# Optimization experiments

Measured on AMD Instinct MI355X. Metric: run time of the kernel, lower is better.

## Reference

```python
import jax, jax.numpy as jnp
import numpy as np

T, B, E, H = 4096, 2, 1024, 16          # seq, batch, embed, heads
W = 256                                  # one-sided attention window (attention_window=512 // 2)
G = 64                                   # number of global tokens (first G positions)
D = E // H
NEG = -1e9


def _band_mask():
    # valid key position for band slot j at query t is t - W + j in [0, T)
    pos = jnp.arange(T)[:, None] - W + jnp.arange(2 * W + 1)[None, :]
    return (pos >= 0) & (pos < T)  # [T, 2W+1]


def _chunk_blocks(x):
    # x: [b, t, h, d] -> key/value blocks [b, nc, 3w, h, d]; block c covers positions [c*w - w, c*w + 2w)
    b, t, h, d = x.shape
    nc = t // W
    xp = jnp.pad(x, ((0, 0), (W, 2 * W), (0, 0), (0, 0)))
    idx = jnp.arange(nc)[:, None] * W + jnp.arange(3 * W)[None, :]
    return xp[:, idx]


def _band_qk(q, k):
    # q,k: [b,t,h,d] -> banded scores [b,t,h,2w+1] (Longformer sliding_chunks_matmul_qk)
    b, t, h, d = q.shape
    nc = t // W
    qc = q.reshape(b, nc, W, h, d)
    kb = _chunk_blocks(k)
    scores = jnp.einsum('bcxhd,bcyhd->bhcxy', qc, kb)          # y in [0, 3w)
    y_idx = jnp.arange(W)[:, None] + jnp.arange(2 * W + 1)[None, :]  # [w, 2w+1]
    band = jnp.take_along_axis(scores, y_idx[None, None, None], axis=-1)
    band = band.reshape(b, h, t, 2 * W + 1).transpose(0, 2, 1, 3)
    return jnp.where(_band_mask()[None, :, None, :], band, NEG)


def _band_pv(p, v):
    # p: [b,t,h,2w+1], v: [b,t,h,d] -> [b,t,h,d] (sliding_chunks_matmul_pv)
    b, t, h, _ = p.shape
    nc = t // W
    pb = p.transpose(0, 2, 1, 3).reshape(b, h, nc, W, 2 * W + 1)
    x = jnp.arange(W)
    y_idx = x[:, None] + jnp.arange(2 * W + 1)[None, :]
    p3 = jnp.zeros((b, h, nc, W, 3 * W), p.dtype).at[:, :, :, x[:, None], y_idx].set(pb)
    vb = _chunk_blocks(v)
    out = jnp.einsum('bhcxy,bcyhd->bcxhd', p3, vb)
    return out.reshape(b, t, h, -1)


def setup_inputs() -> dict:
    key = jax.random.key(0)
    ks = jax.random.split(key, 16)
    s = 0.02
    inp = {
        'query': jax.random.normal(ks[0], (T, B, E), jnp.float32),
        'attn_mask': jnp.concatenate([jnp.ones((B, G), jnp.int64), jnp.zeros((B, T - G), jnp.int64)], axis=1),
        'Wq': jax.random.normal(ks[1], (E, E), jnp.float32) * s, 'bq': jnp.zeros((E,), jnp.float32),
        'Wk': jax.random.normal(ks[2], (E, E), jnp.float32) * s, 'bk': jnp.zeros((E,), jnp.float32),
        'Wv': jax.random.normal(ks[3], (E, E), jnp.float32) * s, 'bv': jnp.zeros((E,), jnp.float32),
        'Wqg': jax.random.normal(ks[4], (E, E), jnp.float32) * s, 'bqg': jnp.zeros((E,), jnp.float32),
        'Wkg': jax.random.normal(ks[5], (E, E), jnp.float32) * s, 'bkg': jnp.zeros((E,), jnp.float32),
        'Wvg': jax.random.normal(ks[6], (E, E), jnp.float32) * s, 'bvg': jnp.zeros((E,), jnp.float32),
        'Wo': jax.random.normal(ks[7], (E, E), jnp.float32) * s, 'bo': jnp.zeros((E,), jnp.float32),
    }
    return inp


def reference(query, attn_mask, Wq, bq, Wk, bk, Wv, bv, Wqg, bqg, Wkg, bkg, Wvg, bvg, Wo, bo):
    del attn_mask  # structure fixed: first G tokens are global, no padding
    scaling = D ** -0.5
    x = query.transpose(1, 0, 2)                      # [b, t, e]
    q = ((x @ Wq.T + bq) * scaling).reshape(B, T, H, D)
    k = (x @ Wk.T + bk).reshape(B, T, H, D)
    v = (x @ Wv.T + bv).reshape(B, T, H, D)

    band = _band_qk(q, k)                             # [b,t,h,2w+1]
    sel_w = jnp.einsum('blhd,bshd->blhs', q, k[:, :G])  # every token attends global keys
    aw = jnp.concatenate([sel_w, band], axis=-1)
    probs = jax.nn.softmax(aw.astype(jnp.float32), axis=-1).astype(aw.dtype)

    attn = jnp.einsum('blhs,bshd->blhd', probs[..., :G], v[:, :G])
    attn = attn + _band_pv(probs[..., G:], v)         # [b,t,h,d]

    # global tokens attend everything with the *_global projections
    qg = ((x[:, :G] @ Wqg.T + bqg) * scaling).reshape(B, G, H, D)
    kg = (x @ Wkg.T + bkg).reshape(B, T, H, D)
    vg = (x @ Wvg.T + bvg).reshape(B, T, H, D)
    gs = jnp.einsum('bghd,bthd->bhgt', qg, kg)
    gp = jax.nn.softmax(gs.astype(jnp.float32), axis=-1).astype(gs.dtype)
    gout = jnp.einsum('bhgt,bthd->bghd', gp, vg)
    attn = attn.at[:, :G].set(gout)

    out = attn.reshape(B, T, E).transpose(1, 0, 2) @ Wo.T + bo  # [t, b, e]
    return out
```

## Files before the change

### kernel.cpp

```cpp
#include <hip/hip_runtime.h>
#include <hip/hip_bf16.h>

typedef unsigned short u16;
typedef __bf16 bf16x8 __attribute__((ext_vector_type(8)));
typedef float  f32x4  __attribute__((ext_vector_type(4)));

constexpr int TT = 4096;
constexpr int BBATCH = 2;
constexpr int EE = 1024;
constexpr int HH = 16;
constexpr int DD = 64;
constexpr int WQ = 256;
constexpr int GG = 64;
constexpr int NSPLIT = 8;

__device__ __forceinline__ u16 f2bf(float f) {
    union { float f; unsigned int i; } c; c.f = f;
    unsigned int x = c.i;
    return (u16)((x + 0x7fffu + ((x >> 16) & 1u)) >> 16);
}
__device__ __forceinline__ uint4 pack8(float4 a, float4 b) {
    uint4 r;
    r.x = (unsigned)f2bf(a.x) | ((unsigned)f2bf(a.y) << 16);
    r.y = (unsigned)f2bf(a.z) | ((unsigned)f2bf(a.w) << 16);
    r.z = (unsigned)f2bf(b.x) | ((unsigned)f2bf(b.y) << 16);
    r.w = (unsigned)f2bf(b.z) | ((unsigned)f2bf(b.w) << 16);
    return r;
}

__device__ __forceinline__ void g2l16(const u16* g, u16* l) {
    __builtin_amdgcn_global_load_lds(
        (const __attribute__((address_space(1))) void*)g,
        (__attribute__((address_space(3))) void*)l, 16, 0, 0);
}

__device__ __forceinline__ void xcd_swizzle(int& bx, int& by) {
    bx = blockIdx.x; by = blockIdx.y;
    if ((gridDim.y & 7) == 0) {
        const int g   = blockIdx.x + blockIdx.y * gridDim.x;
        const int idx = g >> 3;
        bx = idx % gridDim.x;
        by = (g & 7) + ((idx / gridDim.x) << 3);
    }
}

struct WPtrs { const float* p[7]; };
__global__ __launch_bounds__(256) void conv_kernel(
    WPtrs wp, const float* __restrict__ query, u16* __restrict__ wb, u16* __restrict__ xb)
{
    const size_t i8 = ((size_t)blockIdx.x * 256 + threadIdx.x) << 3;
    const size_t WTOT = (size_t)7 << 20;
    const float* src;
    u16* dst;
    if (i8 < WTOT) {
        const int which = (int)(i8 >> 20);
        src = wp.p[which] + (i8 & (((size_t)1 << 20) - 1));
        dst = wb + i8;
    } else {
        const size_t j = i8 - WTOT;
        const size_t e = j & (EE - 1);
        const size_t t = (j >> 10) & (TT - 1);
        const size_t b = j >> 22;
        src = query + (t * BBATCH + b) * EE + e;
        dst = xb + j;
    }
    const float4 f0 = *(const float4*)src;
    const float4 f1 = *(const float4*)(src + 4);
    *(uint4*)dst = pack8(f0, f1);
}

template<int C_F32, int PERMA_QG, int PERMC_TB>
__global__ __launch_bounds__(256) void gemm_kernel(
    const u16* __restrict__ A, const u16* __restrict__ W, const float* __restrict__ bias,
    void* __restrict__ Cv, float scale)
{
    const int tid = threadIdx.x, lane = tid & 63, w = tid >> 6;
    const int wm = w >> 1, wn = w & 1;
    int bx, by;
    xcd_swizzle(bx, by);
    const int m0 = by << 7, n0 = bx << 7;

    __shared__ __align__(16) u16 As[2 * 128 * 32];
    __shared__ __align__(16) u16 Bs[2 * 128 * 32];

    const int lrow = lane >> 2;
    const int lcol = (lane & 3) << 3;
    auto arow = [](int m) -> size_t {
        return PERMA_QG ? (size_t)(((m >> 6) << 12) | (m & 63)) : (size_t)m;
    };
    const u16* gA0 = A + arow(m0 + (w << 4) + lrow) * EE + lcol;
    const u16* gA1 = A + arow(m0 + 64 + (w << 4) + lrow) * EE + lcol;
    const u16* gB0 = W + (size_t)(n0 + (w << 4) + lrow) * EE + lcol;
    const u16* gB1 = gB0 + (size_t)64 * EE;
    u16* lA0 = As + (w << 9);
    u16* lA1 = As + 2048 + (w << 9);
    u16* lB0 = Bs + (w << 9);
    u16* lB1 = Bs + 2048 + (w << 9);

    f32x4 acc[4][4];
#pragma unroll
    for (int i = 0; i < 4; i++)
#pragma unroll
        for (int j = 0; j < 4; j++)
            acc[i][j] = (f32x4){0.f, 0.f, 0.f, 0.f};

    const int fr = lane & 15;
    const int fq = (lane >> 4) << 3;

    for (int k0 = 0; k0 < EE; k0 += 64) {
        g2l16(gA0 + k0, lA0);  g2l16(gA0 + k0 + 32, lA0 + 4096);
        g2l16(gA1 + k0, lA1);  g2l16(gA1 + k0 + 32, lA1 + 4096);
        g2l16(gB0 + k0, lB0);  g2l16(gB0 + k0 + 32, lB0 + 4096);
        g2l16(gB1 + k0, lB1);  g2l16(gB1 + k0 + 32, lB1 + 4096);
        __syncthreads();
#pragma unroll
        for (int p = 0; p < 2; p++) {
            bf16x8 af[4], bfv[4];
#pragma unroll
            for (int i = 0; i < 4; i++)
                af[i] = *(const bf16x8*)&As[p * 4096 + ((wm << 6) + (i << 4) + fr) * 32 + fq];
#pragma unroll
            for (int j = 0; j < 4; j++)
                bfv[j] = *(const bf16x8*)&Bs[p * 4096 + ((wn << 6) + (j << 4) + fr) * 32 + fq];
#pragma unroll
            for (int i = 0; i < 4; i++)
#pragma unroll
                for (int j = 0; j < 4; j++)
                    acc[i][j] = __builtin_amdgcn_mfma_f32_16x16x32_bf16(af[i], bfv[j], acc[i][j], 0, 0, 0);
        }
        __syncthreads();
    }

    const int colbase = n0 + (wn << 6);
    const int rowbase = m0 + (wm << 6) + ((lane >> 4) << 2);
#pragma unroll
    for (int j = 0; j < 4; j++) {
        const int col = colbase + (j << 4) + fr;
        const float bv = bias[col];
#pragma unroll
        for (int i = 0; i < 4; i++) {
#pragma unroll
            for (int r = 0; r < 4; r++) {
                const int row = rowbase + (i << 4) + r;
                const float val = (acc[i][j][r] + bv) * scale;
                const size_t dst = (size_t)(PERMC_TB ? (((row & (TT - 1)) << 1) | (row >> 12)) : row) * EE + col;
                if (C_F32) ((float*)Cv)[dst] = val;
                else       ((u16*)Cv)[dst]   = f2bf(val);
            }
        }
    }
}

struct FusedArgs { u16* out[3]; const float* bias[3]; float scale[3]; int vseg; };
template<int NSEG>
__global__ __launch_bounds__(256) void gemm_fused_kernel(
    const u16* __restrict__ A, const u16* __restrict__ W, FusedArgs fa)
{
    const int tid = threadIdx.x, lane = tid & 63, w = tid >> 6;
    const int wm = w >> 1, wn = w & 1;
    int bx, by;
    xcd_swizzle(bx, by);
    const int m0 = by << 7, n0 = bx << 7;

    __shared__ __align__(16) u16 As[2 * 128 * 32];
    __shared__ __align__(16) u16 Bs[2 * 128 * 32];

    const int lrow = lane >> 2;
    const int lcol = (lane & 3) << 3;
    const u16* gA0 = A + (size_t)(m0 + (w << 4) + lrow) * EE + lcol;
    const u16* gA1 = gA0 + (size_t)64 * EE;
    const u16* gB0 = W + (size_t)(n0 + (w << 4) + lrow) * EE + lcol;
    const u16* gB1 = gB0 + (size_t)64 * EE;
    u16* lA0 = As + (w << 9);
    u16* lA1 = As + 2048 + (w << 9);
    u16* lB0 = Bs + (w << 9);
    u16* lB1 = Bs + 2048 + (w << 9);

    f32x4 acc[4][4];
#pragma unroll
    for (int i = 0; i < 4; i++)
#pragma unroll
        for (int j = 0; j < 4; j++)
            acc[i][j] = (f32x4){0.f, 0.f, 0.f, 0.f};

    const int fr = lane & 15;
    const int fq = (lane >> 4) << 3;

    for (int k0 = 0; k0 < EE; k0 += 64) {
        g2l16(gA0 + k0, lA0);  g2l16(gA0 + k0 + 32, lA0 + 4096);
        g2l16(gA1 + k0, lA1);  g2l16(gA1 + k0 + 32, lA1 + 4096);
        g2l16(gB0 + k0, lB0);  g2l16(gB0 + k0 + 32, lB0 + 4096);
        g2l16(gB1 + k0, lB1);  g2l16(gB1 + k0 + 32, lB1 + 4096);
        __syncthreads();
#pragma unroll
        for (int p = 0; p < 2; p++) {
            bf16x8 af[4], bfv[4];
#pragma unroll
            for (int i = 0; i < 4; i++)
                af[i] = *(const bf16x8*)&As[p * 4096 + ((wm << 6) + (i << 4) + fr) * 32 + fq];
#pragma unroll
            for (int j = 0; j < 4; j++)
                bfv[j] = *(const bf16x8*)&Bs[p * 4096 + ((wn << 6) + (j << 4) + fr) * 32 + fq];
#pragma unroll
            for (int i = 0; i < 4; i++)
#pragma unroll
                for (int j = 0; j < 4; j++)
                    acc[i][j] = __builtin_amdgcn_mfma_f32_16x16x32_bf16(af[i], bfv[j], acc[i][j], 0, 0, 0);
        }
        __syncthreads();
    }

    const int seg = n0 >> 10;
    u16* outp = fa.out[seg];
    const float* bp = fa.bias[seg];
    const float scl = fa.scale[seg];
    const bool vtr = (seg == fa.vseg);

    const int colbase = n0 + (wn << 6);
    const int rowbase = m0 + (wm << 6) + ((lane >> 4) << 2);
#pragma unroll
    for (int j = 0; j < 4; j++) {
        const int col = colbase + (j << 4) + fr;
        const int cl  = col & (EE - 1);
        const float bv = bp[cl];
#pragma unroll
        for (int i = 0; i < 4; i++) {
            if (vtr) {
                const int row0 = rowbase + (i << 4);
                const int bb = row0 >> 12, t = row0 & (TT - 1);
                const int hh = cl >> 6, d = cl & 63;
                ushort4 pk;
                pk.x = f2bf((acc[i][j][0] + bv) * scl);
                pk.y = f2bf((acc[i][j][1] + bv) * scl);
                pk.z = f2bf((acc[i][j][2] + bv) * scl);
                pk.w = f2bf((acc[i][j][3] + bv) * scl);
                *(ushort4*)(outp + (((size_t)(bb * HH + hh) * DD + d) * TT + t)) = pk;
            } else {
#pragma unroll
                for (int r = 0; r < 4; r++) {
                    const int row = rowbase + (i << 4) + r;
                    outp[(size_t)row * EE + cl] = f2bf((acc[i][j][r] + bv) * scl);
                }
            }
        }
    }
}

__global__ __launch_bounds__(256) void band_attn_kernel(
    const u16* __restrict__ q, const u16* __restrict__ k, const u16* __restrict__ vt,
    u16* __restrict__ attnb)
{
    const int tid  = threadIdx.x;
    const int lane = tid & 63;
    const int w    = tid >> 6;
    const int col  = lane & 15;
    const int quad = lane >> 4;

    const int qt = blockIdx.x >> 5;
    const int bh = blockIdx.x & 31;
    const int h  = bh & (HH - 1);
    const int b  = bh >> 4;
    const int t0 = qt << 6;

    __shared__ __align__(16) u16 Ks[64][72];
    __shared__ __align__(16) u16 Vs[64][72];
    __shared__ __align__(16) u16 Ps[4][16][72];

    const size_t base   = (size_t)b * TT * EE + (size_t)h * DD;
    const size_t vtbase = (size_t)bh * DD * TT;

    const u16* qp = q + base + (size_t)(t0 + (w << 4) + col) * EE + (quad << 3);
    const bf16x8 qf0 = *(const bf16x8*)qp;
    const bf16x8 qf1 = *(const bf16x8*)(qp + 32);

    float m_i[4], l_i[4];
    f32x4 acc_o[4];
#pragma unroll
    for (int r = 0; r < 4; r++) { m_i[r] = -1e30f; l_i[r] = 0.f; }
#pragma unroll
    for (int nt = 0; nt < 4; nt++) acc_o[nt] = (f32x4){0.f, 0.f, 0.f, 0.f};

    const int c_lo = 1 + ((t0 < WQ) ? ((WQ - t0) >> 6) : 0);
    const int c_hi = min(9, 1 + ((TT + WQ - 64 - t0) >> 6));

    const int srow  = tid >> 2;
    const int spart = (tid & 3) << 4;

    auto process = [&](int kpos0, int jbase) {
        {
            const u16* ks = k + base + (size_t)(kpos0 + srow) * EE + spart;
            const u16* vs = vt + vtbase + (size_t)srow * TT + kpos0 + spart;
            const uint4 k0v = *(const uint4*)ks;
            const uint4 k1v = *(const uint4*)(ks + 8);
            const uint4 v0v = *(const uint4*)vs;
            const uint4 v1v = *(const uint4*)(vs + 8);
            *(uint4*)&Ks[srow][spart]     = k0v;
            *(uint4*)&Ks[srow][spart + 8] = k1v;
            *(uint4*)&Vs[srow][spart]     = v0v;
            *(uint4*)&Vs[srow][spart + 8] = v1v;
        }
        __syncthreads();

        f32x4 acc_s[4];
#pragma unroll
        for (int nt = 0; nt < 4; nt++) {
            const bf16x8 kf0 = *(const bf16x8*)&Ks[(nt << 4) + col][quad << 3];
            const bf16x8 kf1 = *(const bf16x8*)&Ks[(nt << 4) + col][32 + (quad << 3)];
            f32x4 s = (f32x4){0.f, 0.f, 0.f, 0.f};
            s = __builtin_amdgcn_mfma_f32_16x16x32_bf16(qf0, kf0, s, 0, 0, 0);
            s = __builtin_amdgcn_mfma_f32_16x16x32_bf16(qf1, kf1, s, 0, 0, 0);
            acc_s[nt] = s;
        }

        if (jbase >= 0) {
#pragma unroll
            for (int nt = 0; nt < 4; nt++) {
#pragma unroll
                for (int r = 0; r < 4; r++) {
                    const int jp   = jbase + (nt << 4) + col;
                    const int qrow = (w << 4) + (quad << 2) + r;
                    const bool ok  = (jp >= qrow) && (jp <= qrow + 2 * WQ);
                    if (!ok) acc_s[nt][r] = -1e30f;
                }
            }
        }

        float p_sum[4];
#pragma unroll
        for (int r = 0; r < 4; r++) {
            float mx = fmaxf(fmaxf(acc_s[0][r], acc_s[1][r]), fmaxf(acc_s[2][r], acc_s[3][r]));
#pragma unroll
            for (int off = 1; off < 16; off <<= 1) mx = fmaxf(mx, __shfl_xor(mx, off));
            const float m_new = fmaxf(m_i[r], mx);
            const float alpha = __expf(m_i[r] - m_new);
            m_i[r] = m_new;
            l_i[r] *= alpha;
#pragma unroll
            for (int nt = 0; nt < 4; nt++) acc_o[nt][r] *= alpha;
            float ps = 0.f;
#pragma unroll
            for (int nt = 0; nt < 4; nt++) {
                const float e = __expf(acc_s[nt][r] - m_new);
                acc_s[nt][r] = e;
                ps += e;
            }
            p_sum[r] = ps;
        }
#pragma unroll
        for (int r = 0; r < 4; r++) {
            float ps = p_sum[r];
#pragma unroll
            for (int off = 1; off < 16; off <<= 1) ps += __shfl_xor(ps, off);
            l_i[r] += ps;
        }

#pragma unroll
        for (int nt = 0; nt < 4; nt++)
#pragma unroll
            for (int r = 0; r < 4; r++)
                Ps[w][(quad << 2) + r][(nt << 4) + col] = f2bf(acc_s[nt][r]);

        const bf16x8 pf0 = *(const bf16x8*)&Ps[w][col][quad << 3];
        const bf16x8 pf1 = *(const bf16x8*)&Ps[w][col][32 + (quad << 3)];

#pragma unroll
        for (int nt = 0; nt < 4; nt++) {
            const bf16x8 vf0 = *(const bf16x8*)&Vs[(nt << 4) + col][quad << 3];
            const bf16x8 vf1 = *(const bf16x8*)&Vs[(nt << 4) + col][32 + (quad << 3)];
            acc_o[nt] = __builtin_amdgcn_mfma_f32_16x16x32_bf16(pf0, vf0, acc_o[nt], 0, 0, 0);
            acc_o[nt] = __builtin_amdgcn_mfma_f32_16x16x32_bf16(pf1, vf1, acc_o[nt], 0, 0, 0);
        }
        __syncthreads();
    };

    process(0, -1);
#pragma unroll 1
    for (int c = c_lo; c <= c_hi; c++) {
        const int kpos0 = t0 - WQ + ((c - 1) << 6);
        const bool edge = (c == 1) || (c == 9);
        process(kpos0, edge ? ((c - 1) << 6) : -1);
    }

    float inv[4];
#pragma unroll
    for (int r = 0; r < 4; r++) inv[r] = 1.f / l_i[r];
#pragma unroll
    for (int nt = 0; nt < 4; nt++) {
#pragma unroll
        for (int r = 0; r < 4; r++) {
            const int t = t0 + (w << 4) + (quad << 2) + r;
            attnb[base + (size_t)t * EE + (nt << 4) + col] = f2bf(acc_o[nt][r] * inv[r]);
        }
    }
}

__global__ __launch_bounds__(256) void global_attn_flash_kernel(
    const u16* __restrict__ qg, const u16* __restrict__ kg, const u16* __restrict__ vg,
    float* __restrict__ Op, float* __restrict__ Ml, float* __restrict__ Ll)
{
    const int tid  = threadIdx.x;
    const int lane = tid & 63;
    const int w    = tid >> 6;
    const int col  = lane & 15;
    const int quad = lane >> 4;

    const int s  = blockIdx.x & (NSPLIT - 1);
    const int h  = (blockIdx.x >> 3) & (HH - 1);
    const int b  = blockIdx.x >> 7;
    const int k0pos = s * (TT / NSPLIT);

    __shared__ __align__(16) u16 Qs[64][72];
    __shared__ __align__(16) u16 Ks[64][72];
    __shared__ __align__(16) u16 Vs[64][70];
    __shared__ __align__(16) u16 Ps[4][16][72];

    const size_t base = (size_t)b * TT * EE + (size_t)h * DD;

    {
        const int qr   = tid >> 2;
        const int part = (tid & 3) << 4;
        const uint4* src = (const uint4*)(qg + (size_t)(b * GG + qr) * EE + (size_t)h * DD + part);
        *(uint4*)&Qs[qr][part]     = src[0];
        *(uint4*)&Qs[qr][part + 8] = src[1];
    }

    float m_i[4], l_i[4];
    f32x4 acc_o[4];
#pragma unroll
    for (int r = 0; r < 4; r++) { m_i[r] = -1e30f; l_i[r] = 0.f; }
#pragma unroll
    for (int nt = 0; nt < 4; nt++) acc_o[nt] = (f32x4){0.f, 0.f, 0.f, 0.f};

#pragma unroll 1
    for (int cc = 0; cc < TT / NSPLIT / 64; cc++) {
        {
            const int kk   = tid >> 2;
            const int part = (tid & 3) << 4;
            const int pos  = k0pos + (cc << 6) + kk;
            const uint4* ks = (const uint4*)(kg + base + (size_t)pos * EE + part);
            const uint4* vs = (const uint4*)(vg + base + (size_t)pos * EE + part);
            const uint4 k0v = ks[0], k1v = ks[1];
            const uint4 v0v = vs[0], v1v = vs[1];
            *(uint4*)&Ks[kk][part]     = k0v;
            *(uint4*)&Ks[kk][part + 8] = k1v;
            unsigned int* vd = (unsigned int*)&Vs[kk][part];
            vd[0] = v0v.x; vd[1] = v0v.y; vd[2] = v0v.z; vd[3] = v0v.w;
            vd[4] = v1v.x; vd[5] = v1v.y; vd[6] = v1v.z; vd[7] = v1v.w;
        }
        __syncthreads();

        bf16x8 qf0 = *(const bf16x8*)&Qs[(w << 4) + col][quad << 3];
        bf16x8 qf1 = *(const bf16x8*)&Qs[(w << 4) + col][32 + (quad << 3)];
        f32x4 acc_s[4];
#pragma unroll
        for (int nt = 0; nt < 4; nt++) {
            bf16x8 kf0 = *(const bf16x8*)&Ks[(nt << 4) + col][quad << 3];
            bf16x8 kf1 = *(const bf16x8*)&Ks[(nt << 4) + col][32 + (quad << 3)];
            f32x4 sv = (f32x4){0.f, 0.f, 0.f, 0.f};
            sv = __builtin_amdgcn_mfma_f32_16x16x32_bf16(qf0, kf0, sv, 0, 0, 0);
            sv = __builtin_amdgcn_mfma_f32_16x16x32_bf16(qf1, kf1, sv, 0, 0, 0);
            acc_s[nt] = sv;
        }

        float m_c[4], p_sum[4];
#pragma unroll
        for (int r = 0; r < 4; r++) {
            float mx = fmaxf(fmaxf(acc_s[0][r], acc_s[1][r]), fmaxf(acc_s[2][r], acc_s[3][r]));
#pragma unroll
            for (int off = 1; off < 16; off <<= 1) mx = fmaxf(mx, __shfl_xor(mx, off));
            m_c[r] = mx;
        }
#pragma unroll
        for (int r = 0; r < 4; r++) {
            const float m_new = fmaxf(m_i[r], m_c[r]);
            const float alpha = __expf(m_i[r] - m_new);
            m_i[r] = m_new;
            l_i[r] *= alpha;
#pragma unroll
            for (int nt = 0; nt < 4; nt++) acc_o[nt][r] *= alpha;
            float ps = 0.f;
#pragma unroll
            for (int nt = 0; nt < 4; nt++) {
                const float e = __expf(acc_s[nt][r] - m_new);
                acc_s[nt][r] = e;
                ps += e;
            }
            p_sum[r] = ps;
        }
#pragma unroll
        for (int r = 0; r < 4; r++) {
            float ps = p_sum[r];
#pragma unroll
            for (int off = 1; off < 16; off <<= 1) ps += __shfl_xor(ps, off);
            l_i[r] += ps;
        }

#pragma unroll
        for (int nt = 0; nt < 4; nt++)
#pragma unroll
            for (int r = 0; r < 4; r++)
                Ps[w][(quad << 2) + r][(nt << 4) + col] = f2bf(acc_s[nt][r]);

        bf16x8 pf0 = *(const bf16x8*)&Ps[w][col][quad << 3];
        bf16x8 pf1 = *(const bf16x8*)&Ps[w][col][32 + (quad << 3)];
#pragma unroll
        for (int nt = 0; nt < 4; nt++) {
            union { bf16x8 v; u16 e[8]; } vf0, vf1;
#pragma unroll
            for (int j = 0; j < 8; j++) {
                vf0.e[j] = Vs[(quad << 3) + j][(nt << 4) + col];
                vf1.e[j] = Vs[32 + (quad << 3) + j][(nt << 4) + col];
            }
            acc_o[nt] = __builtin_amdgcn_mfma_f32_16x16x32_bf16(pf0, vf0.v, acc_o[nt], 0, 0, 0);
            acc_o[nt] = __builtin_amdgcn_mfma_f32_16x16x32_bf16(pf1, vf1.v, acc_o[nt], 0, 0, 0);
        }
        __syncthreads();
    }

    const size_t obase = (size_t)blockIdx.x * GG * DD;
#pragma unroll
    for (int nt = 0; nt < 4; nt++) {
#pragma unroll
        for (int r = 0; r < 4; r++) {
            const int row = (w << 4) + (quad << 2) + r;
            Op[obase + (size_t)row * DD + (nt << 4) + col] = acc_o[nt][r];
        }
    }
    if (col == 0) {
#pragma unroll
        for (int r = 0; r < 4; r++) {
            const int row = (w << 4) + (quad << 2) + r;
            Ml[blockIdx.x * GG + row] = m_i[r];
            Ll[blockIdx.x * GG + row] = l_i[r];
        }
    }
}

__global__ __launch_bounds__(256) void global_combine_kernel(
    const float* __restrict__ Op, const float* __restrict__ Ml, const float* __restrict__ Ll,
    u16* __restrict__ attnb)
{
    const int bh  = blockIdx.x;
    const int b   = bh >> 4;
    const int h   = bh & (HH - 1);
    const int row = threadIdx.x >> 2;
    const int d0  = (threadIdx.x & 3) << 4;

    float mv[NSPLIT];
    float m = -1e30f;
#pragma unroll
    for (int s = 0; s < NSPLIT; s++) {
        mv[s] = Ml[(bh * NSPLIT + s) * GG + row];
        m = fmaxf(m, mv[s]);
    }
    float l = 0.f;
    float sc[NSPLIT];
#pragma unroll
    for (int s = 0; s < NSPLIT; s++) {
        sc[s] = __expf(mv[s] - m);
        l += Ll[(bh * NSPLIT + s) * GG + row] * sc[s];
    }
    float o[16];
#pragma unroll
    for (int j = 0; j < 16; j++) o[j] = 0.f;
#pragma unroll
    for (int s = 0; s < NSPLIT; s++) {
        const float* src = Op + ((size_t)(bh * NSPLIT + s) * GG + row) * DD + d0;
        const float f = sc[s];
#pragma unroll
        for (int j = 0; j < 16; j += 4) {
            const float4 v4 = *(const float4*)(src + j);
            o[j + 0] = fmaf(v4.x, f, o[j + 0]);
            o[j + 1] = fmaf(v4.y, f, o[j + 1]);
            o[j + 2] = fmaf(v4.z, f, o[j + 2]);
            o[j + 3] = fmaf(v4.w, f, o[j + 3]);
        }
    }
    const float inv = 1.f / l;
    u16* dst = attnb + ((size_t)b * TT + row) * EE + (size_t)h * DD + d0;
#pragma unroll
    for (int j = 0; j < 16; j++) dst[j] = f2bf(o[j] * inv);
}

extern "C" void kernel_launch(void* const* d_in, const int* in_sizes, int n_in,
                              void* d_out, int out_size, void* d_ws, size_t ws_size,
                              hipStream_t stream)
{
    (void)in_sizes; (void)n_in; (void)out_size; (void)ws_size;
    const float* query = (const float*)d_in[0];
    const float* Wq  = (const float*)d_in[2];  const float* bq  = (const float*)d_in[3];
    const float* Wk  = (const float*)d_in[4];  const float* bk  = (const float*)d_in[5];
    const float* Wv  = (const float*)d_in[6];  const float* bv  = (const float*)d_in[7];
    const float* Wqg = (const float*)d_in[8];  const float* bqg = (const float*)d_in[9];
    const float* Wkg = (const float*)d_in[10]; const float* bkg = (const float*)d_in[11];
    const float* Wvg = (const float*)d_in[12]; const float* bvg = (const float*)d_in[13];
    const float* Wo  = (const float*)d_in[14]; const float* bo  = (const float*)d_in[15];

    const size_t nfull = (size_t)BBATCH * TT * EE;
    const size_t wsz   = (size_t)1 << 20;
    u16* xb    = (u16*)d_ws;
    u16* wb    = xb + nfull;
    u16* slotA = wb + 7 * wsz;
    u16* slotB = slotA + nfull;
    u16* slotC = slotB + nfull;
    u16* qg    = slotC + nfull;
    float* Op  = (float*)(qg + (size_t)BBATCH * GG * EE);
    float* Ml  = Op + (size_t)BBATCH * HH * NSPLIT * GG * DD;
    float* Ll  = Ml + (size_t)BBATCH * HH * NSPLIT * GG;
    u16* attnb = xb;

    WPtrs wp;
    wp.p[0] = Wq; wp.p[1] = Wk; wp.p[2] = Wv;
    wp.p[3] = Wkg; wp.p[4] = Wvg; wp.p[5] = Wqg; wp.p[6] = Wo;

    const dim3 blk(256);
    const dim3 gF2(16, 64);
    const dim3 gF3(24, 64);
    const dim3 gFull(8, 64);
    const dim3 gQg(8, 1);
    const float sc = 0.125f;

    conv_kernel<<<7680, blk, 0, stream>>>(wp, query, wb, xb);

    gemm_kernel<0, 1, 0><<<gQg, blk, 0, stream>>>(xb, wb + 5 * wsz, bqg, qg, sc);

    FusedArgs fa2;
    fa2.out[0] = slotA; fa2.out[1] = slotB; fa2.out[2] = nullptr;
    fa2.bias[0] = bkg;  fa2.bias[1] = bvg;  fa2.bias[2] = nullptr;
    fa2.scale[0] = 1.f; fa2.scale[1] = 1.f; fa2.scale[2] = 1.f;
    fa2.vseg = -1;
    gemm_fused_kernel<2><<<gF2, blk, 0, stream>>>(xb, wb + 3 * wsz, fa2);
    global_attn_flash_kernel<<<BBATCH * HH * NSPLIT, blk, 0, stream>>>(qg, slotA, slotB, Op, Ml, Ll);

    FusedArgs fa3;
    fa3.out[0] = slotA; fa3.out[1] = slotB; fa3.out[2] = slotC;
    fa3.bias[0] = bq;   fa3.bias[1] = bk;   fa3.bias[2] = bv;
    fa3.scale[0] = sc;  fa3.scale[1] = 1.f; fa3.scale[2] = 1.f;
    fa3.vseg = 2;
    gemm_fused_kernel<3><<<gF3, blk, 0, stream>>>(xb, wb, fa3);

    band_attn_kernel<<<BBATCH * HH * (TT / 64), blk, 0, stream>>>(slotA, slotB, slotC, attnb);
    global_combine_kernel<<<BBATCH * HH, blk, 0, stream>>>(Op, Ml, Ll, attnb);

    gemm_kernel<1, 0, 1><<<gFull, blk, 0, stream>>>(attnb, wb + 6 * wsz, bo, (void*)d_out, 1.f);
}
```

Before: 375.9 us.

## Double-buffer GEMM LDS tiles with XOR swizzle and split-phase prefetch

Replaces the fused projection GEMM with a double-buffered kernel. It prefetches the next K tile's A and B halves into the alternate LDS buffer while MFMAs run on the current one, uses an XOR-swizzled LDS layout to cut bank conflicts, and raises MFMA wave priority with s_setprio. The output projection now also uses this kernel through new fp32-output and row-permute template flags. The cost is doubled LDS (64KB per block) with a 2-blocks-per-CU launch bound and more barriers per iteration.

Result: faster. 366.0 us (-2.6%).

```diff
diff --git a/kernel.cpp b/kernel.cpp
--- a/kernel.cpp
+++ b/kernel.cpp
@@ -152,8 +152,9 @@
 }
 
 struct FusedArgs { u16* out[3]; const float* bias[3]; float scale[3]; int vseg; };
-template<int NSEG>
-__global__ __launch_bounds__(256) void gemm_fused_kernel(
+
+template<int NSEG, int CF32, int PERMC>
+__global__ __launch_bounds__(256, 2) void gemm_pipe_kernel(
     const u16* __restrict__ A, const u16* __restrict__ W, FusedArgs fa)
 {
     const int tid = threadIdx.x, lane = tid & 63, w = tid >> 6;
@@ -162,19 +163,15 @@
     xcd_swizzle(bx, by);
     const int m0 = by << 7, n0 = bx << 7;
 
-    __shared__ __align__(16) u16 As[2 * 128 * 32];
-    __shared__ __align__(16) u16 Bs[2 * 128 * 32];
-
-    const int lrow = lane >> 2;
-    const int lcol = (lane & 3) << 3;
-    const u16* gA0 = A + (size_t)(m0 + (w << 4) + lrow) * EE + lcol;
-    const u16* gA1 = gA0 + (size_t)64 * EE;
-    const u16* gB0 = W + (size_t)(n0 + (w << 4) + lrow) * EE + lcol;
-    const u16* gB1 = gB0 + (size_t)64 * EE;
-    u16* lA0 = As + (w << 9);
-    u16* lA1 = As + 2048 + (w << 9);
-    u16* lB0 = Bs + (w << 9);
-    u16* lB1 = Bs + 2048 + (w << 9);
+    __shared__ __align__(16) u16 As[2][8192];
+    __shared__ __align__(16) u16 Bs[2][8192];
+
+    const int srow = lane >> 3;
+    const int scol = ((lane & 7) ^ srow) << 3;
+    const u16* gA = A + (size_t)(m0 + (w << 5) + srow) * EE + scol;
+    const u16* gB = W + (size_t)(n0 + (w << 5) + srow) * EE + scol;
+    u16* lA = &As[0][0] + (w << 11);
+    u16* lB = &Bs[0][0] + (w << 11);
 
     f32x4 acc[4][4];
 #pragma unroll
@@ -184,37 +181,76 @@
             acc[i][j] = (f32x4){0.f, 0.f, 0.f, 0.f};
 
     const int fr = lane & 15;
-    const int fq = (lane >> 4) << 3;
-
-    for (int k0 = 0; k0 < EE; k0 += 64) {
-        g2l16(gA0 + k0, lA0);  g2l16(gA0 + k0 + 32, lA0 + 4096);
-        g2l16(gA1 + k0, lA1);  g2l16(gA1 + k0 + 32, lA1 + 4096);
-        g2l16(gB0 + k0, lB0);  g2l16(gB0 + k0 + 32, lB0 + 4096);
-        g2l16(gB1 + k0, lB1);  g2l16(gB1 + k0 + 32, lB1 + 4096);
+    const int qb = (lane >> 4) << 4;
+    const int xr = (fr & 7) << 4;
+
+    auto stageA = [&](int k0, int buf) {
+#pragma unroll
+        for (int l = 0; l < 4; l++)
+            g2l16(gA + (size_t)(l << 3) * EE + k0, lA + buf * 8192 + (l << 9));
+    };
+    auto stageB = [&](int k0, int buf) {
+#pragma unroll
+        for (int l = 0; l < 4; l++)
+            g2l16(gB + (size_t)(l << 3) * EE + k0, lB + buf * 8192 + (l << 9));
+    };
+
+    stageA(0, 0);
+    stageB(0, 0);
+    __syncthreads();
+
+    constexpr int NT = EE / 64;
+#pragma unroll 2
+    for (int t = 0; t < NT; t++) {
+        const int buf = t & 1;
+        const bool pf = (t + 1 < NT);
+        const int kn = (t + 1) << 6;
+        bf16x8 af[4], bfv[4];
+
+#pragma unroll
+        for (int mi = 0; mi < 4; mi++)
+            af[mi] = *(const bf16x8*)((const char*)&As[buf][0] +
+                      ((((wm << 6) + (mi << 4) + fr)) << 7) + (qb ^ xr));
+#pragma unroll
+        for (int nj = 0; nj < 4; nj++)
+            bfv[nj] = *(const bf16x8*)((const char*)&Bs[buf][0] +
+                      ((((wn << 6) + (nj << 4) + fr)) << 7) + (qb ^ xr));
+        if (pf) stageA(kn, buf ^ 1);
+        __builtin_amdgcn_s_barrier();
+        __builtin_amdgcn_s_setprio(1);
+#pragma unroll
+        for (int mi = 0; mi < 4; mi++)
+#pragma unroll
+            for (int nj = 0; nj < 4; nj++)
+                acc[mi][nj] = __builtin_amdgcn_mfma_f32_16x16x32_bf16(af[mi], bfv[nj], acc[mi][nj], 0, 0, 0);
+        __builtin_amdgcn_s_setprio(0);
+        __builtin_amdgcn_s_barrier();
+
+#pragma unroll
+        for (int mi = 0; mi < 4; mi++)
+            af[mi] = *(const bf16x8*)((const char*)&As[buf][0] +
+                      ((((wm << 6) + (mi << 4) + fr)) << 7) + ((64 | qb) ^ xr));
+#pragma unroll
+        for (int nj = 0; nj < 4; nj++)
+            bfv[nj] = *(const bf16x8*)((const char*)&Bs[buf][0] +
+                      ((((wn << 6) + (nj << 4) + fr)) << 7) + ((64 | qb) ^ xr));
+        if (pf) stageB(kn, buf ^ 1);
+        __builtin_amdgcn_s_barrier();
+        __builtin_amdgcn_s_setprio(1);
+#pragma unroll
+        for (int mi = 0; mi < 4; mi++)
+#pragma unroll
+            for (int nj = 0; nj < 4; nj++)
+                acc[mi][nj] = __builtin_amdgcn_mfma_f32_16x16x32_bf16(af[mi], bfv[nj], acc[mi][nj], 0, 0, 0);
+        __builtin_amdgcn_s_setprio(0);
         __syncthreads();
-#pragma unroll
-        for (int p = 0; p < 2; p++) {
-            bf16x8 af[4], bfv[4];
-#pragma unroll
-            for (int i = 0; i < 4; i++)
-                af[i] = *(const bf16x8*)&As[p * 4096 + ((wm << 6) + (i << 4) + fr) * 32 + fq];
-#pragma unroll
-            for (int j = 0; j < 4; j++)
-                bfv[j] = *(const bf16x8*)&Bs[p * 4096 + ((wn << 6) + (j << 4) + fr) * 32 + fq];
-#pragma unroll
-            for (int i = 0; i < 4; i++)
-#pragma unroll
-                for (int j = 0; j < 4; j++)
-                    acc[i][j] = __builtin_amdgcn_mfma_f32_16x16x32_bf16(af[i], bfv[j], acc[i][j], 0, 0, 0);
-        }
-        __syncthreads();
-    }
-
-    const int seg = n0 >> 10;
+    }
+
+    const int seg = (NSEG > 1) ? (n0 >> 10) : 0;
     u16* outp = fa.out[seg];
     const float* bp = fa.bias[seg];
     const float scl = fa.scale[seg];
-    const bool vtr = (seg == fa.vseg);
+    const bool vtr = (NSEG > 1) && (seg == fa.vseg);
 
     const int colbase = n0 + (wn << 6);
     const int rowbase = m0 + (wm << 6) + ((lane >> 4) << 2);
@@ -239,7 +275,11 @@
 #pragma unroll
                 for (int r = 0; r < 4; r++) {
                     const int row = rowbase + (i << 4) + r;
-                    outp[(size_t)row * EE + cl] = f2bf((acc[i][j][r] + bv) * scl);
+                    const float val = (acc[i][j][r] + bv) * scl;
+                    const size_t drow = PERMC ? (size_t)(((row & (TT - 1)) << 1) | (row >> 12))
+                                              : (size_t)row;
+                    if (CF32) ((float*)outp)[drow * EE + cl] = val;
+                    else      outp[drow * EE + cl] = f2bf(val);
                 }
             }
         }
@@ -629,7 +669,7 @@
     fa2.bias[0] = bkg;  fa2.bias[1] = bvg;  fa2.bias[2] = nullptr;
     fa2.scale[0] = 1.f; fa2.scale[1] = 1.f; fa2.scale[2] = 1.f;
     fa2.vseg = -1;
-    gemm_fused_kernel<2><<<gF2, blk, 0, stream>>>(xb, wb + 3 * wsz, fa2);
+    gemm_pipe_kernel<2, 0, 0><<<gF2, blk, 0, stream>>>(xb, wb + 3 * wsz, fa2);
     global_attn_flash_kernel<<<BBATCH * HH * NSPLIT, blk, 0, stream>>>(qg, slotA, slotB, Op, Ml, Ll);
 
     FusedArgs fa3;
@@ -637,10 +677,15 @@
     fa3.bias[0] = bq;   fa3.bias[1] = bk;   fa3.bias[2] = bv;
     fa3.scale[0] = sc;  fa3.scale[1] = 1.f; fa3.scale[2] = 1.f;
     fa3.vseg = 2;
-    gemm_fused_kernel<3><<<gF3, blk, 0, stream>>>(xb, wb, fa3);
+    gemm_pipe_kernel<3, 0, 0><<<gF3, blk, 0, stream>>>(xb, wb, fa3);
 
     band_attn_kernel<<<BBATCH * HH * (TT / 64), blk, 0, stream>>>(slotA, slotB, slotC, attnb);
     global_combine_kernel<<<BBATCH * HH, blk, 0, stream>>>(Op, Ml, Ll, attnb);
 
-    gemm_kernel<1, 0, 1><<<gFull, blk, 0, stream>>>(attnb, wb + 6 * wsz, bo, (void*)d_out, 1.f);
-}
+    FusedArgs faO;
+    faO.out[0] = (u16*)d_out; faO.out[1] = nullptr; faO.out[2] = nullptr;
+    faO.bias[0] = bo;         faO.bias[1] = nullptr; faO.bias[2] = nullptr;
+    faO.scale[0] = 1.f;       faO.scale[1] = 1.f;    faO.scale[2] = 1.f;
+    faO.vseg = -1;
+    gemm_pipe_kernel<1, 1, 1><<<gFull, blk, 0, stream>>>(attnb, wb + 6 * wsz, faO);
+}
```
